# Kernel optimization log

Hardware: AMD Instinct MI355X
Metric: run time of the kernel (lower is better)

Reference implementation:

```python
import jax, jax.numpy as jnp
import numpy as np

N_NODES = 100000
N_EDGES = 600000
N_GRAPHS = 256
K = 5
N_FEAT = 16
N_CLASSES = 4


def setup_inputs() -> dict:
    key = jax.random.key(0)
    ks = jax.random.split(key, 12)
    x = jax.random.normal(ks[0], (N_NODES, N_FEAT), dtype=jnp.float32)
    edge_index = jax.random.randint(ks[1], (2, N_EDGES), 0, N_NODES, dtype=jnp.int32)
    batch = jnp.sort(jax.random.randint(ks[2], (N_NODES,), 0, N_GRAPHS, dtype=jnp.int32))
    s = 0.1
    W11 = jax.random.normal(ks[3], (K, N_FEAT, 64), dtype=jnp.float32) * s
    b11 = jnp.zeros((64,), dtype=jnp.float32)
    W12 = jax.random.normal(ks[4], (K, N_FEAT, 64), dtype=jnp.float32) * s
    b12 = jnp.zeros((64,), dtype=jnp.float32)
    W21 = jax.random.normal(ks[5], (K, 128, 256), dtype=jnp.float32) * s
    b21 = jnp.zeros((256,), dtype=jnp.float32)
    W22 = jax.random.normal(ks[6], (K, 128, 256), dtype=jnp.float32) * s
    b22 = jnp.zeros((256,), dtype=jnp.float32)
    fc_w = jax.random.normal(ks[7], (512, N_CLASSES), dtype=jnp.float32) * s
    fc_b = jnp.zeros((N_CLASSES,), dtype=jnp.float32)
    return {
        "x": x, "edge_index": edge_index, "batch": batch,
        "W11": W11, "b11": b11, "W12": W12, "b12": b12,
        "W21": W21, "b21": b21, "W22": W22, "b22": b22,
        "fc_w": fc_w, "fc_b": fc_b,
    }


def _cheb_norm(src, dst, n_nodes):
    # PyG ChebConv (sym norm, lambda_max=2): L_hat = -D^{-1/2} A D^{-1/2},
    # zero diagonal. Degree computed over source (row) indices.
    deg = jax.ops.segment_sum(jnp.ones_like(src, dtype=jnp.float32), src,
                              num_segments=n_nodes)
    dinv = jnp.where(deg > 0, jax.lax.rsqrt(jnp.maximum(deg, 1.0)), 0.0)
    return -dinv[src] * dinv[dst]


def _cheb_conv(x, src, dst, w_norm, W, b):
    # Chebyshev recursion: Tx0=x, Tx1=L_hat x, Txk = 2 L_hat Tx_{k-1} - Tx_{k-2}
    n = x.shape[0]

    def spmm(h):  # aggregate messages from src at dst
        return jax.ops.segment_sum(h[src] * w_norm[:, None], dst, num_segments=n)

    Tx0 = x
    Tx1 = spmm(x)
    out = jnp.einsum('nf,fo->no', Tx0, W[0]) + jnp.einsum('nf,fo->no', Tx1, W[1])
    for k in range(2, W.shape[0]):
        Tx2 = 2.0 * spmm(Tx1) - Tx0
        out = out + jnp.einsum('nf,fo->no', Tx2, W[k])
        Tx0, Tx1 = Tx1, Tx2
    return out + b


def reference(x, edge_index, batch, W11, b11, W12, b12, W21, b21, W22, b22,
              fc_w, fc_b):
    src, dst = edge_index[0], edge_index[1]
    w_fwd = _cheb_norm(src, dst, N_NODES)
    w_rev = _cheb_norm(dst, src, N_NODES)  # reversed adjacency

    x1 = jax.nn.relu(_cheb_conv(x, src, dst, w_fwd, W11, b11))
    x2 = jax.nn.relu(_cheb_conv(x, dst, src, w_rev, W12, b12))
    h = jnp.concatenate([x1, x2], axis=1)  # [N, 128]

    x1 = jax.nn.relu(_cheb_conv(h, src, dst, w_fwd, W21, b21))
    x2 = jax.nn.relu(_cheb_conv(h, dst, src, w_rev, W22, b22))
    h = jnp.concatenate([x1, x2], axis=1)  # [N, 512]

    # global mean pool over graphs
    sums = jax.ops.segment_sum(h, batch, num_segments=N_GRAPHS)
    cnt = jax.ops.segment_sum(jnp.ones((h.shape[0],), dtype=h.dtype), batch,
                              num_segments=N_GRAPHS)
    pooled = sums / jnp.maximum(cnt, 1.0)[:, None]  # [G, 512]

    logits = pooled @ fc_w + fc_b
    return jax.nn.log_softmax(logits, axis=1)
```

## Files before the change

### kernel.cpp

```cpp
#include <hip/hip_runtime.h>
#include <stdint.h>

#define NNODES 100000
#define NEDGES 600000
#define NGRAPH 256
#define KCH 5
#define F1 16
#define O1 64
#define F2 128
#define O2 256
#define FT1 (KCH * F1)
#define FT2 (KCH * F2)
#define STR2 512
#define KSTEPS 20
#define KS1 3
#define LROW 40
#define LROWD 68
#define NXCD 8

typedef unsigned short ushort_t;
typedef __attribute__((ext_vector_type(8))) short bf16x8;
typedef __attribute__((ext_vector_type(4))) float f32x4;

__device__ __forceinline__ float bflo(unsigned int u) {
    union { unsigned int u; float f; } v; v.u = u << 16; return v.f;
}
__device__ __forceinline__ float bfhi(unsigned int u) {
    union { unsigned int u; float f; } v; v.u = u & 0xFFFF0000u; return v.f;
}
__device__ __forceinline__ unsigned int f2bf(float f) {
    union { float f; unsigned int u; } v; v.f = f;
    return (v.u + 0x7FFFu + ((v.u >> 16) & 1u)) >> 16;
}
__device__ __forceinline__ unsigned int pack2(float lo, float hi) {
    return (f2bf(hi) << 16) | f2bf(lo);
}


__global__ void k_count(const int* __restrict__ src, const int* __restrict__ dst,
                        int* __restrict__ cntDst, int* __restrict__ cntSrc, int E) {
    int e = blockIdx.x * 256 + threadIdx.x;
    if (e < E) {
        atomicAdd(&cntDst[dst[e]], 1);
        atomicAdd(&cntSrc[src[e]], 1);
    }
}

__global__ void k_dinv(const int* __restrict__ cntDst, const int* __restrict__ cntSrc,
                       float* __restrict__ dinvF, float* __restrict__ dinvR, int n) {
    int i = blockIdx.x * 256 + threadIdx.x;
    if (i < n) {
        int cs = cntSrc[i], cd = cntDst[i];
        dinvF[i] = cs > 0 ? rsqrtf((float)cs) : 0.f;
        dinvR[i] = cd > 0 ? rsqrtf((float)cd) : 0.f;
    }
}

__global__ void k_scan1m(const int* __restrict__ inF, int* __restrict__ outF,
                         int* __restrict__ bsF,
                         const int* __restrict__ inR, int* __restrict__ outR,
                         int* __restrict__ bsR, int n, int NB) {
    __shared__ int a[512];
    __shared__ int s[256];
    int b = blockIdx.x;
    const int* in; int* out; int* bs; int lb;
    if (b < NB) { in = inF; out = outF; bs = bsF; lb = b; }
    else        { in = inR; out = outR; bs = bsR; lb = b - NB; }
    int t = threadIdx.x;
    int base = lb * 512;
    a[t]       = (base + t < n)       ? in[base + t]       : 0;
    a[t + 256] = (base + t + 256 < n) ? in[base + t + 256] : 0;
    __syncthreads();
    s[t] = a[2 * t] + a[2 * t + 1];
    __syncthreads();
    for (int off = 1; off < 256; off <<= 1) {
        int v = (t >= off) ? s[t - off] : 0;
        __syncthreads();
        s[t] += v;
        __syncthreads();
    }
    int ep = (t > 0) ? s[t - 1] : 0;
    if (base + 2 * t < n)     out[base + 2 * t]     = ep;
    if (base + 2 * t + 1 < n) out[base + 2 * t + 1] = ep + a[2 * t];
    if (t == 255) bs[lb] = s[255];
}

__global__ void k_scan2m(int* __restrict__ bsF, int* __restrict__ bsR, int nb) {
    __shared__ int s[256];
    int* bs = (blockIdx.x == 0) ? bsF : bsR;
    int t = threadIdx.x;
    s[t] = (t < nb) ? bs[t] : 0;
    __syncthreads();
    for (int off = 1; off < 256; off <<= 1) {
        int v = (t >= off) ? s[t - off] : 0;
        __syncthreads();
        s[t] += v;
        __syncthreads();
    }
    if (t < nb) bs[t] = (t > 0) ? s[t - 1] : 0;
}

__global__ void k_scan3m(int* __restrict__ outF, int* __restrict__ curF,
                         const int* __restrict__ bsF,
                         int* __restrict__ outR, int* __restrict__ curR,
                         const int* __restrict__ bsR, int n, int E, int NB) {
    int b = blockIdx.x;
    int* out; int* cur; const int* bs; int lb;
    if (b < NB) { out = outF; cur = curF; bs = bsF; lb = b; }
    else        { out = outR; cur = curR; bs = bsR; lb = b - NB; }
    int i = lb * 512 + threadIdx.x;
    int add = bs[lb];
    if (i < n)       { int v = out[i] + add;       out[i] = v;       cur[i] = v; }
    if (i + 256 < n) { int v = out[i + 256] + add; out[i + 256] = v; cur[i + 256] = v; }
    if (lb == 0 && threadIdx.x == 0) out[n] = E;
}

__global__ void k_scatter(const int* __restrict__ src, const int* __restrict__ dst,
                          const float* __restrict__ dinvF, const float* __restrict__ dinvR,
                          int* __restrict__ curF, int* __restrict__ curR,
                          int2* __restrict__ edF, int2* __restrict__ edR, int E,
                          int chunk) {
    int c = blockIdx.x & (NXCD - 1);
    int sb = blockIdx.x >> 3;
    int slices = gridDim.x >> 3;
    int lo = c * chunk, hi = lo + chunk;
    for (int e = sb * 256 + threadIdx.x; e < E; e += slices * 256) {
        int s = src[e], d = dst[e];
        if (d >= lo && d < hi) {
            int p = atomicAdd(&curF[d], 1);
            float wf = -dinvF[s] * dinvF[d];
            edF[p] = make_int2(s, __float_as_int(wf));
        }
        if (s >= lo && s < hi) {
            int q = atomicAdd(&curR[s], 1);
            float wr = -dinvR[s] * dinvR[d];
            edR[q] = make_int2(d, __float_as_int(wr));
        }
    }
}

__global__ void k_gstart(const int* __restrict__ batch, int* __restrict__ gstart, int n) {
    int g = blockIdx.x * 64 + threadIdx.x;
    if (g > NGRAPH) return;
    if (g == NGRAPH) { gstart[g] = n; return; }
    int lo = 0, hi = n;
    while (lo < hi) {
        int mid = (lo + hi) >> 1;
        if (batch[mid] < g) lo = mid + 1; else hi = mid;
    }
    gstart[g] = lo;
}


__global__ void k_copyx(const float* __restrict__ x, float* __restrict__ Tx,
                        ushort_t* __restrict__ TxB, int n) {
    int tid = blockIdx.x * 256 + threadIdx.x;
    int r = tid >> 2, c = tid & 3;
    if (r < n) {
        float4 v = *(const float4*)(x + (size_t)r * 16 + c * 4);
        *(float4*)(Tx + (size_t)r * FT1 + c * 4) = v;
        uint2 b;
        b.x = pack2(v.x, v.y);
        b.y = pack2(v.z, v.w);
        *(uint2*)(TxB + (size_t)r * F1 + c * 4) = b;
    }
}

__global__ void k_spmm_f32(const ushort_t* __restrict__ HinB, float* __restrict__ Hout,
                           ushort_t* __restrict__ HoutB,
                           const float* __restrict__ Tx0,
                           const int* __restrict__ off, const int2* __restrict__ ed,
                           int n) {
    int tid = blockIdx.x * 256 + threadIdx.x;
    int r = tid >> 2, c = tid & 3;
    if (r >= n) return;
    int j0 = off[r], j1 = off[r + 1];
    float4 s = {0.f, 0.f, 0.f, 0.f};
    int j = j0;
    for (; j + 4 <= j1; j += 4) {
        int2 e0 = ed[j], e1 = ed[j + 1], e2 = ed[j + 2], e3 = ed[j + 3];
        float wa = __int_as_float(e0.y), wb = __int_as_float(e1.y);
        float wc = __int_as_float(e2.y), wd = __int_as_float(e3.y);
        const uint2 h0 = *(const uint2*)(HinB + (size_t)e0.x * F1 + c * 4);
        const uint2 h1 = *(const uint2*)(HinB + (size_t)e1.x * F1 + c * 4);
        const uint2 h2 = *(const uint2*)(HinB + (size_t)e2.x * F1 + c * 4);
        const uint2 h3 = *(const uint2*)(HinB + (size_t)e3.x * F1 + c * 4);
        s.x = fmaf(wa, bflo(h0.x), s.x); s.y = fmaf(wa, bfhi(h0.x), s.y);
        s.z = fmaf(wa, bflo(h0.y), s.z); s.w = fmaf(wa, bfhi(h0.y), s.w);
        s.x = fmaf(wb, bflo(h1.x), s.x); s.y = fmaf(wb, bfhi(h1.x), s.y);
        s.z = fmaf(wb, bflo(h1.y), s.z); s.w = fmaf(wb, bfhi(h1.y), s.w);
        s.x = fmaf(wc, bflo(h2.x), s.x); s.y = fmaf(wc, bfhi(h2.x), s.y);
        s.z = fmaf(wc, bflo(h2.y), s.z); s.w = fmaf(wc, bfhi(h2.y), s.w);
        s.x = fmaf(wd, bflo(h3.x), s.x); s.y = fmaf(wd, bfhi(h3.x), s.y);
        s.z = fmaf(wd, bflo(h3.y), s.z); s.w = fmaf(wd, bfhi(h3.y), s.w);
    }
    for (; j < j1; ++j) {
        int2 e = ed[j];
        float w2 = __int_as_float(e.y);
        const uint2 h = *(const uint2*)(HinB + (size_t)e.x * F1 + c * 4);
        s.x = fmaf(w2, bflo(h.x), s.x); s.y = fmaf(w2, bfhi(h.x), s.y);
        s.z = fmaf(w2, bflo(h.y), s.z); s.w = fmaf(w2, bfhi(h.y), s.w);
    }
    float4 o;
    if (Tx0) {
        const float4 t0 = *(const float4*)(Tx0 + (size_t)r * FT1 + c * 4);
        o.x = 2.f * s.x - t0.x; o.y = 2.f * s.y - t0.y;
        o.z = 2.f * s.z - t0.z; o.w = 2.f * s.w - t0.w;
    } else {
        o = s;
    }
    *(float4*)(Hout + (size_t)r * FT1 + c * 4) = o;
    if (HoutB) {
        uint2 b;
        b.x = pack2(o.x, o.y);
        b.y = pack2(o.z, o.w);
        *(uint2*)(HoutB + (size_t)r * F1 + c * 4) = b;
    }
}

__global__ void k_spmm_bf(const ushort_t* __restrict__ Hin, ushort_t* __restrict__ Hout,
                          const ushort_t* __restrict__ Tx0,
                          const int* __restrict__ off, const int2* __restrict__ ed,
                          int n) {
    int r = blockIdx.x * 4 + (threadIdx.x >> 6);
    r = __builtin_amdgcn_readfirstlane(r);
    int c = threadIdx.x & 63;
    if (r >= n) return;
    int j0 = __builtin_amdgcn_readfirstlane(off[r]);
    int j1 = __builtin_amdgcn_readfirstlane(off[r + 1]);
    float s0 = 0.f, s1 = 0.f;
    int j = j0;
    int jfull = j0 + ((j1 - j0) & ~7);
    for (; j < jfull; j += 8) {
        float w[8];
        unsigned int h[8];
#pragma unroll
        for (int sl = 0; sl < 8; ++sl) {
            int2 e = ed[j + sl];
            w[sl] = __int_as_float(e.y);
            h[sl] = *(const unsigned int*)(Hin + (size_t)e.x * STR2 + c * 2);
        }
#pragma unroll
        for (int sl = 0; sl < 8; ++sl) {
            s0 = fmaf(bflo(h[sl]), w[sl], s0);
            s1 = fmaf(bfhi(h[sl]), w[sl], s1);
        }
    }
    int rem = j1 - j;
    if (rem) {
        float w[8];
        unsigned int h[8];
#pragma unroll
        for (int sl = 0; sl < 8; ++sl) {
            w[sl] = 0.f; h[sl] = 0u;
            if (sl < rem) {
                int2 e = ed[j + sl];
                w[sl] = __int_as_float(e.y);
                h[sl] = *(const unsigned int*)(Hin + (size_t)e.x * STR2 + c * 2);
            }
        }
#pragma unroll
        for (int sl = 0; sl < 8; ++sl) {
            s0 = fmaf(bflo(h[sl]), w[sl], s0);
            s1 = fmaf(bfhi(h[sl]), w[sl], s1);
        }
    }
    if (Tx0) {
        unsigned int t0 = *(const unsigned int*)(Tx0 + (size_t)r * STR2 + c * 2);
        s0 = 2.f * s0 - bflo(t0);
        s1 = 2.f * s1 - bfhi(t0);
    }
    *(unsigned int*)(Hout + (size_t)r * STR2 + c * 2) = pack2(s0, s1);
}

__global__ void k_packW1m(const float* __restrict__ WF, ushort_t* __restrict__ BpF_,
                          const float* __restrict__ WR, ushort_t* __restrict__ BpR_) {
    int b = blockIdx.x;
    const float* W = (b < 3) ? WF : WR;
    ushort_t* Bp = (b < 3) ? BpF_ : BpR_;
    int tid = ((b < 3) ? b : b - 3) * 256 + threadIdx.x;
    if (tid >= 4 * KS1 * 64) return;
    int lane = tid & 63;
    int ks = (tid >> 6) % KS1;
    int nt = tid / (64 * KS1);
    int k0 = ks * 32 + (lane >> 4) * 8;
    int ncol = nt * 16 + (lane & 15);
    float v[8];
#pragma unroll
    for (int j = 0; j < 8; ++j) {
        int k = k0 + j;
        v[j] = (k < FT1) ? W[(size_t)k * O1 + ncol] : 0.f;
    }
    uint4 o;
    o.x = pack2(v[0], v[1]); o.y = pack2(v[2], v[3]);
    o.z = pack2(v[4], v[5]); o.w = pack2(v[6], v[7]);
    *(uint4*)(Bp + (size_t)tid * 8) = o;
}

__global__ __launch_bounds__(256) void k_gemm1_mfma(
    const float* __restrict__ A, const ushort_t* __restrict__ Bp,
    const float* __restrict__ bias, ushort_t* __restrict__ out, int n) {
    int lane = threadIdx.x & 63;
    int wvi = threadIdx.x >> 6;
    int mrow = lane & 15;
    int quad = lane >> 4;
    int m0w = blockIdx.x * 64 + wvi * 16;
    int row = m0w + mrow;
    int rowc = row < n ? row : n - 1;
    const float* Ar = A + (size_t)rowc * FT1 + quad * 8;

    f32x4 acc[4] = {};
#pragma unroll
    for (int ks = 0; ks < KS1; ++ks) {
        float4 a0 = *(const float4*)(Ar + ks * 32);
        float4 a1 = *(const float4*)(Ar + ks * 32 + 4);
        union { bf16x8 v; unsigned int u[4]; } ua;
        ua.u[0] = pack2(a0.x, a0.y);
        ua.u[1] = pack2(a0.z, a0.w);
        ua.u[2] = pack2(a1.x, a1.y);
        ua.u[3] = pack2(a1.z, a1.w);
#pragma unroll
        for (int nf = 0; nf < 4; ++nf) {
            bf16x8 bfr = *(const bf16x8*)(Bp + ((size_t)(nf * KS1 + ks) * 64 + lane) * 8);
            acc[nf] = __builtin_amdgcn_mfma_f32_16x16x32_bf16(ua.v, bfr, acc[nf], 0, 0, 0);
        }
    }
#pragma unroll
    for (int nf = 0; nf < 4; ++nf) {
        float bb = bias[nf * 16 + mrow];
#pragma unroll
        for (int reg = 0; reg < 4; ++reg) {
            int orow = m0w + quad * 4 + reg;
            if (orow < n)
                out[(size_t)orow * STR2 + nf * 16 + mrow] =
                    (ushort_t)f2bf(fmaxf(acc[nf][reg] + bb, 0.f));
        }
    }
}

__global__ void k_packWm(const float* __restrict__ WF, ushort_t* __restrict__ BpF_,
                         const float* __restrict__ WR, ushort_t* __restrict__ BpR_) {
    int b = blockIdx.x;
    const float* W = (b < 80) ? WF : WR;
    ushort_t* Bp = (b < 80) ? BpF_ : BpR_;
    int tid = ((b < 80) ? b : b - 80) * 256 + threadIdx.x;
    if (tid >= 16 * KSTEPS * 64) return;
    int lane = tid & 63;
    int ks = (tid >> 6) % KSTEPS;
    int nt = tid / (64 * KSTEPS);
    int k0 = ks * 32 + (lane >> 4) * 8;
    int ncol = nt * 16 + (lane & 15);
    float v[8];
#pragma unroll
    for (int j = 0; j < 8; ++j) v[j] = W[(size_t)(k0 + j) * O2 + ncol];
    uint4 o;
    o.x = pack2(v[0], v[1]); o.y = pack2(v[2], v[3]);
    o.z = pack2(v[4], v[5]); o.w = pack2(v[6], v[7]);
    *(uint4*)(Bp + (size_t)tid * 8) = o;
}

__global__ __launch_bounds__(256) void k_spmm4_gemm(
    const ushort_t* __restrict__ Hin,
    const ushort_t* __restrict__ Txc,
    const int* __restrict__ off, const int2* __restrict__ ed,
    const ushort_t* __restrict__ A,
    const ushort_t* __restrict__ Bp,
    const float* __restrict__ bias, float* __restrict__ pooled, int colofs,
    const int* __restrict__ batch, int n) {
    __shared__ ushort_t lds[2][64 * LROW];
    __shared__ unsigned int a4[64 * LROWD];

    int lane = threadIdx.x & 63;
    int wv = threadIdx.x >> 6;
    int m0 = blockIdx.x * 64;

    for (int i = 0; i < 16; ++i) {
        int r = m0 + wv * 16 + i;
        float s0 = 0.f, s1 = 0.f;
        if (r < n) {
            int j0 = __builtin_amdgcn_readfirstlane(off[r]);
            int j1 = __builtin_amdgcn_readfirstlane(off[r + 1]);
            int j = j0;
            int jfull = j0 + ((j1 - j0) & ~7);
            for (; j < jfull; j += 8) {
                float w[8];
                unsigned int h[8];
#pragma unroll
                for (int sl = 0; sl < 8; ++sl) {
                    int2 e = ed[j + sl];
                    w[sl] = __int_as_float(e.y);
                    h[sl] = *(const unsigned int*)(Hin + (size_t)e.x * STR2 + lane * 2);
                }
#pragma unroll
                for (int sl = 0; sl < 8; ++sl) {
                    s0 = fmaf(bflo(h[sl]), w[sl], s0);
                    s1 = fmaf(bfhi(h[sl]), w[sl], s1);
                }
            }
            int rem = j1 - j;
            if (rem) {
                float w[8];
                unsigned int h[8];
#pragma unroll
                for (int sl = 0; sl < 8; ++sl) {
                    w[sl] = 0.f; h[sl] = 0u;
                    if (sl < rem) {
                        int2 e = ed[j + sl];
                        w[sl] = __int_as_float(e.y);
                        h[sl] = *(const unsigned int*)(Hin + (size_t)e.x * STR2 + lane * 2);
                    }
                }
#pragma unroll
                for (int sl = 0; sl < 8; ++sl) {
                    s0 = fmaf(bflo(h[sl]), w[sl], s0);
                    s1 = fmaf(bfhi(h[sl]), w[sl], s1);
                }
            }
            unsigned int t0 = *(const unsigned int*)(Txc + (size_t)r * STR2 + lane * 2);
            s0 = 2.f * s0 - bflo(t0);
            s1 = 2.f * s1 - bfhi(t0);
        }
        a4[(wv * 16 + i) * LROWD + lane] = pack2(s0, s1);
    }
    __syncthreads();

    int mrow = lane & 15;
    int quad = lane >> 4;
    int srow = threadIdx.x >> 2;
    int sc = threadIdx.x & 3;

    const ushort_t* Ag = A + (size_t)(m0 + srow) * STR2 + sc * 8;
    const ushort_t* Bbase = Bp + ((size_t)(wv * 4) * KSTEPS * 64 + lane) * 8;
    int sidx = srow * LROW + sc * 8;

    f32x4 acc[4][4] = {};
    uint4 nxt;
    bf16x8 bcur[4], bnxt[4];
    {
        uint4 c0 = *(const uint4*)(Ag);
        *(uint4*)&lds[0][sidx] = c0;
        nxt = *(const uint4*)(Ag + 32);
#pragma unroll
        for (int nf = 0; nf < 4; ++nf)
            bcur[nf] = *(const bf16x8*)(Bbase + ((size_t)nf * KSTEPS) * 512);
    }

    for (int ks = 0; ks < KSTEPS; ++ks) {
        __syncthreads();
        if (ks + 1 < 16)
            *(uint4*)&lds[(ks + 1) & 1][sidx] = nxt;
        if (ks + 2 < 16)
            nxt = *(const uint4*)(Ag + (ks + 2) * 32);
        if (ks + 1 < KSTEPS) {
#pragma unroll
            for (int nf = 0; nf < 4; ++nf)
                bnxt[nf] = *(const bf16x8*)(Bbase + ((size_t)nf * KSTEPS + ks + 1) * 512);
        }
        bf16x8 af[4];
        if (ks < 16) {
            const ushort_t* lbuf = &lds[ks & 1][0];
#pragma unroll
            for (int mf = 0; mf < 4; ++mf)
                af[mf] = *(const bf16x8*)(lbuf + (mf * 16 + mrow) * LROW + quad * 8);
        } else {
            int kk = ks - 16;
#pragma unroll
            for (int mf = 0; mf < 4; ++mf)
                af[mf] = *(const bf16x8*)(a4 + (size_t)(mf * 16 + mrow) * LROWD +
                                          kk * 16 + quad * 4);
        }
#pragma unroll
        for (int mf = 0; mf < 4; ++mf)
#pragma unroll
            for (int nf = 0; nf < 4; ++nf)
                acc[mf][nf] = __builtin_amdgcn_mfma_f32_16x16x32_bf16(
                    af[mf], bcur[nf], acc[mf][nf], 0, 0, 0);
#pragma unroll
        for (int nf = 0; nf < 4; ++nf) bcur[nf] = bnxt[nf];
    }

    float bcol[4];
#pragma unroll
    for (int nf = 0; nf < 4; ++nf) bcol[nf] = bias[wv * 64 + nf * 16 + mrow];

#pragma unroll
    for (int mf = 0; mf < 4; ++mf) {
        int t0 = m0 + mf * 16;
        if (t0 >= n) break;
        int te = (t0 + 15 < n) ? t0 + 15 : n - 1;
        int r0 = t0 + quad * 4;
        if (batch[t0] == batch[te]) {
            int g = batch[t0];
#pragma unroll
            for (int nf = 0; nf < 4; ++nf) {
                float s = 0.f;
#pragma unroll
                for (int reg = 0; reg < 4; ++reg) {
                    float v = fmaxf(acc[mf][nf][reg] + bcol[nf], 0.f);
                    if (r0 + reg < n) s += v;
                }
                s += __shfl_xor(s, 16, 64);
                s += __shfl_xor(s, 32, 64);
                if (quad == 0)
                    atomicAdd(pooled + (size_t)g * 512 + colofs + wv * 64 + nf * 16 + mrow, s);
            }
        } else {
            int gb[4];
#pragma unroll
            for (int reg = 0; reg < 4; ++reg)
                gb[reg] = batch[(r0 + reg < n) ? r0 + reg : n - 1];
#pragma unroll
            for (int nf = 0; nf < 4; ++nf) {
                int col = colofs + wv * 64 + nf * 16 + mrow;
                float run = 0.f;
                int g = gb[0];
                bool any = false;
#pragma unroll
                for (int reg = 0; reg < 4; ++reg) {
                    int row = r0 + reg;
                    if (row >= n) break;
                    float v = fmaxf(acc[mf][nf][reg] + bcol[nf], 0.f);
                    if (gb[reg] != g) {
                        atomicAdd(pooled + (size_t)g * 512 + col, run);
                        run = 0.f;
                        g = gb[reg];
                    }
                    run += v;
                    any = true;
                }
                if (any) atomicAdd(pooled + (size_t)g * 512 + col, run);
            }
        }
    }
}

__global__ void k_logits(const float* __restrict__ pooled, const int* __restrict__ gstart,
                         const float* __restrict__ fcw, const float* __restrict__ fcb,
                         float* __restrict__ out) {
    int g = blockIdx.x;
    int l = threadIdx.x;
    int cnt = gstart[g + 1] - gstart[g];
    float inv = 1.f / (float)(cnt > 1 ? cnt : 1);
    float lg0 = 0.f, lg1 = 0.f, lg2 = 0.f, lg3 = 0.f;
    for (int f = l; f < 512; f += 64) {
        float p = pooled[g * 512 + f] * inv;
        const float4 wv4 = *(const float4*)(fcw + f * 4);
        lg0 = fmaf(p, wv4.x, lg0);
        lg1 = fmaf(p, wv4.y, lg1);
        lg2 = fmaf(p, wv4.z, lg2);
        lg3 = fmaf(p, wv4.w, lg3);
    }
#pragma unroll
    for (int o = 32; o > 0; o >>= 1) {
        lg0 += __shfl_down(lg0, o, 64);
        lg1 += __shfl_down(lg1, o, 64);
        lg2 += __shfl_down(lg2, o, 64);
        lg3 += __shfl_down(lg3, o, 64);
    }
    if (l == 0) {
        float lg[4] = {lg0 + fcb[0], lg1 + fcb[1], lg2 + fcb[2], lg3 + fcb[3]};
        float m = fmaxf(fmaxf(lg[0], lg[1]), fmaxf(lg[2], lg[3]));
        float s = 0.f;
#pragma unroll
        for (int o = 0; o < 4; ++o) s += expf(lg[o] - m);
        float lsum = logf(s);
#pragma unroll
        for (int o = 0; o < 4; ++o) out[g * 4 + o] = lg[o] - m - lsum;
    }
}


extern "C" void kernel_launch(void* const* d_in, const int* in_sizes, int n_in,
                              void* d_out, int out_size, void* d_ws, size_t ws_size,
                              hipStream_t stream) {
    const float* x   = (const float*)d_in[0];
    const int* ei    = (const int*)d_in[1];
    const int* batch = (const int*)d_in[2];
    const float* W11 = (const float*)d_in[3];
    const float* b11 = (const float*)d_in[4];
    const float* W12 = (const float*)d_in[5];
    const float* b12 = (const float*)d_in[6];
    const float* W21 = (const float*)d_in[7];
    const float* b21 = (const float*)d_in[8];
    const float* W22 = (const float*)d_in[9];
    const float* b22 = (const float*)d_in[10];
    const float* fcw = (const float*)d_in[11];
    const float* fcb = (const float*)d_in[12];
    float* out = (float*)d_out;

    const int N = in_sizes[0] / F1;
    const int E = in_sizes[1] / 2;
    const int* src = ei;
    const int* dst = ei + E;

    char* w = (char*)d_ws;
    size_t pos = 0;
    auto alloc = [&](size_t bytes) -> void* {
        void* p = w + pos;
        pos += (bytes + 255) & ~(size_t)255;
        return p;
    };
    int* cur_f   = (int*)alloc((size_t)N * 4);
    int* cur_r   = (int*)alloc((size_t)N * 4);
    int* off_f   = (int*)alloc((size_t)(N + 1) * 4);
    int* off_r   = (int*)alloc((size_t)(N + 1) * 4);
    float* dinvF = (float*)alloc((size_t)N * 4);
    float* dinvR = (float*)alloc((size_t)N * 4);
    int2* ed_f   = (int2*)alloc((size_t)E * 8);
    int2* ed_r   = (int2*)alloc((size_t)E * 8);
    int* blks_f  = (int*)alloc(1024);
    int* blks_r  = (int*)alloc(1024);
    int* gstart  = (int*)alloc((NGRAPH + 1) * 4);
    float* pooled = (float*)alloc((size_t)NGRAPH * 512 * 4);
    ushort_t* BpF = (ushort_t*)alloc((size_t)FT2 * O2 * 2);
    ushort_t* BpR = (ushort_t*)alloc((size_t)FT2 * O2 * 2);
    ushort_t* Bp1F = (ushort_t*)alloc((size_t)4 * KS1 * 64 * 8 * 2);
    ushort_t* Bp1R = (ushort_t*)alloc((size_t)4 * KS1 * 64 * 8 * 2);
    float* TxAll1 = (float*)alloc(((size_t)N * FT1 + 256) * 4);
    ushort_t* TxB1 = (ushort_t*)alloc((size_t)KCH * N * F1 * 2);
    ushort_t* TxAll2 = (ushort_t*)alloc((size_t)(N + 64) * STR2 * 2);

    (void)hipMemsetAsync(cur_f, 0, (size_t)N * 4, stream);
    (void)hipMemsetAsync(cur_r, 0, (size_t)N * 4, stream);
    (void)hipMemsetAsync(pooled, 0, (size_t)NGRAPH * 512 * 4, stream);

    int gE = (E + 255) / 256, gN = (N + 255) / 256;
    k_count<<<gE, 256, 0, stream>>>(src, dst, cur_f, cur_r, E);
    k_dinv<<<gN, 256, 0, stream>>>(cur_f, cur_r, dinvF, dinvR, N);

    int NB = (N + 511) / 512;
    k_scan1m<<<2 * NB, 256, 0, stream>>>(cur_f, off_f, blks_f, cur_r, off_r, blks_r, N, NB);
    k_scan2m<<<2, 256, 0, stream>>>(blks_f, blks_r, NB);
    k_scan3m<<<2 * NB, 256, 0, stream>>>(off_f, cur_f, blks_f, off_r, cur_r, blks_r, N, E, NB);
    int chunk = (N + NXCD - 1) / NXCD;
    k_scatter<<<NXCD * 256, 256, 0, stream>>>(src, dst, dinvF, dinvR, cur_f, cur_r,
                                              ed_f, ed_r, E, chunk);
    k_gstart<<<5, 64, 0, stream>>>(batch, gstart, N);
    k_packWm<<<160, 256, 0, stream>>>(W21, BpF, W22, BpR);
    k_packW1m<<<6, 256, 0, stream>>>(W11, Bp1F, W12, Bp1R);

    k_copyx<<<(N * 4 + 255) / 256, 256, 0, stream>>>(x, TxAll1, TxB1, N);
    int gs1 = (N * 4 + 255) / 256;
    int gg1 = (N + 63) / 64;
    auto C1 = [&](int k) { return TxAll1 + k * F1; };
    auto B1 = [&](int k) { return TxB1 + (size_t)k * N * F1; };
    k_spmm_f32<<<gs1, 256, 0, stream>>>(B1(0), C1(1), B1(1), nullptr, off_f, ed_f, N);
    k_spmm_f32<<<gs1, 256, 0, stream>>>(B1(1), C1(2), B1(2), C1(0), off_f, ed_f, N);
    k_spmm_f32<<<gs1, 256, 0, stream>>>(B1(2), C1(3), B1(3), C1(1), off_f, ed_f, N);
    k_spmm_f32<<<gs1, 256, 0, stream>>>(B1(3), C1(4), nullptr, C1(2), off_f, ed_f, N);
    k_gemm1_mfma<<<gg1, 256, 0, stream>>>(TxAll1, Bp1F, b11, TxAll2, N);
    k_spmm_f32<<<gs1, 256, 0, stream>>>(B1(0), C1(1), B1(1), nullptr, off_r, ed_r, N);
    k_spmm_f32<<<gs1, 256, 0, stream>>>(B1(1), C1(2), B1(2), C1(0), off_r, ed_r, N);
    k_spmm_f32<<<gs1, 256, 0, stream>>>(B1(2), C1(3), B1(3), C1(1), off_r, ed_r, N);
    k_spmm_f32<<<gs1, 256, 0, stream>>>(B1(3), C1(4), nullptr, C1(2), off_r, ed_r, N);
    k_gemm1_mfma<<<gg1, 256, 0, stream>>>(TxAll1, Bp1R, b12, TxAll2 + O1, N);

    int gs2 = (N + 3) / 4;
    auto C2 = [&](int k) { return TxAll2 + k * F2; };
    int gg = (N + 63) / 64;
    k_spmm_bf<<<gs2, 256, 0, stream>>>(C2(0), C2(1), nullptr, off_f, ed_f, N);
    k_spmm_bf<<<gs2, 256, 0, stream>>>(C2(1), C2(2), C2(0), off_f, ed_f, N);
    k_spmm_bf<<<gs2, 256, 0, stream>>>(C2(2), C2(3), C2(1), off_f, ed_f, N);
    k_spmm4_gemm<<<gg, 256, 0, stream>>>(C2(3), C2(2), off_f, ed_f, TxAll2, BpF,
                                         b21, pooled, 0, batch, N);
    k_spmm_bf<<<gs2, 256, 0, stream>>>(C2(0), C2(1), nullptr, off_r, ed_r, N);
    k_spmm_bf<<<gs2, 256, 0, stream>>>(C2(1), C2(2), C2(0), off_r, ed_r, N);
    k_spmm_bf<<<gs2, 256, 0, stream>>>(C2(2), C2(3), C2(1), off_r, ed_r, N);
    k_spmm4_gemm<<<gg, 256, 0, stream>>>(C2(3), C2(2), off_r, ed_r, TxAll2, BpR,
                                         b22, pooled, 256, batch, N);

    k_logits<<<NGRAPH, 64, 0, stream>>>(pooled, gstart, fcw, fcb, out);
}
```

Baseline: 854.8 us.

## Batch forward and reverse Chebyshev branches into dual-direction kernel launches

Forward and reverse Chebyshev branches now run in shared launches: blockIdx selects direction, which doubles the grid and halves the launch count. Layer-2 features move to separate H (stride 128) and per-direction C buffers, and the fused spmm4+gemm becomes a plain spmm followed by a GEMM that reads H and C. Layer-1 spmm now gathers fp32 directly instead of a bf16 shadow copy. This adds workspace (a second C buffer) and a serial fallback path, and drops the spmm4-in-GEMM fusion, which costs an extra write and read of Tx4.

```diff
diff --git a/kernel.cpp b/kernel.cpp
--- a/kernel.cpp
+++ b/kernel.cpp
@@ -1,8 +1,6 @@
 #include <hip/hip_runtime.h>
 #include <stdint.h>
 
-#define NNODES 100000
-#define NEDGES 600000
 #define NGRAPH 256
 #define KCH 5
 #define F1 16
@@ -11,11 +9,11 @@
 #define O2 256
 #define FT1 (KCH * F1)
 #define FT2 (KCH * F2)
-#define STR2 512
+#define STRH 128
+#define STRC 512
 #define KSTEPS 20
 #define KS1 3
 #define LROW 40
-#define LROWD 68
 #define NXCD 8
 
 typedef unsigned short ushort_t;
@@ -152,26 +150,30 @@
 }
 
 
-__global__ void k_copyx(const float* __restrict__ x, float* __restrict__ Tx,
-                        ushort_t* __restrict__ TxB, int n) {
+__global__ void k_copyx(const float* __restrict__ x, float* __restrict__ TxF,
+                        float* __restrict__ TxR, int n) {
     int tid = blockIdx.x * 256 + threadIdx.x;
     int r = tid >> 2, c = tid & 3;
     if (r < n) {
         float4 v = *(const float4*)(x + (size_t)r * 16 + c * 4);
-        *(float4*)(Tx + (size_t)r * FT1 + c * 4) = v;
-        uint2 b;
-        b.x = pack2(v.x, v.y);
-        b.y = pack2(v.z, v.w);
-        *(uint2*)(TxB + (size_t)r * F1 + c * 4) = b;
-    }
-}
-
-__global__ void k_spmm_f32(const ushort_t* __restrict__ HinB, float* __restrict__ Hout,
-                           ushort_t* __restrict__ HoutB,
-                           const float* __restrict__ Tx0,
-                           const int* __restrict__ off, const int2* __restrict__ ed,
-                           int n) {
-    int tid = blockIdx.x * 256 + threadIdx.x;
+        *(float4*)(TxF + (size_t)r * FT1 + c * 4) = v;
+        if (TxR) *(float4*)(TxR + (size_t)r * FT1 + c * 4) = v;
+    }
+}
+
+__global__ void k_spmm_f32d(const float* __restrict__ HinF, float* __restrict__ HoutF,
+                            const float* __restrict__ Tx0F,
+                            const float* __restrict__ HinR, float* __restrict__ HoutR,
+                            const float* __restrict__ Tx0R,
+                            const int* __restrict__ offF, const int2* __restrict__ edF,
+                            const int* __restrict__ offR, const int2* __restrict__ edR,
+                            int n, int half) {
+    int b = blockIdx.x;
+    const float* Hin; float* Hout; const float* Tx0;
+    const int* off; const int2* ed; int lb;
+    if (b < half) { Hin = HinF; Hout = HoutF; Tx0 = Tx0F; off = offF; ed = edF; lb = b; }
+    else          { Hin = HinR; Hout = HoutR; Tx0 = Tx0R; off = offR; ed = edR; lb = b - half; }
+    int tid = lb * 256 + threadIdx.x;
     int r = tid >> 2, c = tid & 3;
     if (r >= n) return;
     int j0 = off[r], j1 = off[r + 1];
@@ -181,25 +183,20 @@
         int2 e0 = ed[j], e1 = ed[j + 1], e2 = ed[j + 2], e3 = ed[j + 3];
         float wa = __int_as_float(e0.y), wb = __int_as_float(e1.y);
         float wc = __int_as_float(e2.y), wd = __int_as_float(e3.y);
-        const uint2 h0 = *(const uint2*)(HinB + (size_t)e0.x * F1 + c * 4);
-        const uint2 h1 = *(const uint2*)(HinB + (size_t)e1.x * F1 + c * 4);
-        const uint2 h2 = *(const uint2*)(HinB + (size_t)e2.x * F1 + c * 4);
-        const uint2 h3 = *(const uint2*)(HinB + (size_t)e3.x * F1 + c * 4);
-        s.x = fmaf(wa, bflo(h0.x), s.x); s.y = fmaf(wa, bfhi(h0.x), s.y);
-        s.z = fmaf(wa, bflo(h0.y), s.z); s.w = fmaf(wa, bfhi(h0.y), s.w);
-        s.x = fmaf(wb, bflo(h1.x), s.x); s.y = fmaf(wb, bfhi(h1.x), s.y);
-        s.z = fmaf(wb, bflo(h1.y), s.z); s.w = fmaf(wb, bfhi(h1.y), s.w);
-        s.x = fmaf(wc, bflo(h2.x), s.x); s.y = fmaf(wc, bfhi(h2.x), s.y);
-        s.z = fmaf(wc, bflo(h2.y), s.z); s.w = fmaf(wc, bfhi(h2.y), s.w);
-        s.x = fmaf(wd, bflo(h3.x), s.x); s.y = fmaf(wd, bfhi(h3.x), s.y);
-        s.z = fmaf(wd, bflo(h3.y), s.z); s.w = fmaf(wd, bfhi(h3.y), s.w);
+        const float4 h0 = *(const float4*)(Hin + (size_t)e0.x * FT1 + c * 4);
+        const float4 h1 = *(const float4*)(Hin + (size_t)e1.x * FT1 + c * 4);
+        const float4 h2 = *(const float4*)(Hin + (size_t)e2.x * FT1 + c * 4);
+        const float4 h3 = *(const float4*)(Hin + (size_t)e3.x * FT1 + c * 4);
+        s.x += wa * h0.x; s.y += wa * h0.y; s.z += wa * h0.z; s.w += wa * h0.w;
+        s.x += wb * h1.x; s.y += wb * h1.y; s.z += wb * h1.z; s.w += wb * h1.w;
+        s.x += wc * h2.x; s.y += wc * h2.y; s.z += wc * h2.z; s.w += wc * h2.w;
+        s.x += wd * h3.x; s.y += wd * h3.y; s.z += wd * h3.z; s.w += wd * h3.w;
     }
     for (; j < j1; ++j) {
         int2 e = ed[j];
         float w2 = __int_as_float(e.y);
-        const uint2 h = *(const uint2*)(HinB + (size_t)e.x * F1 + c * 4);
-        s.x = fmaf(w2, bflo(h.x), s.x); s.y = fmaf(w2, bfhi(h.x), s.y);
-        s.z = fmaf(w2, bflo(h.y), s.z); s.w = fmaf(w2, bfhi(h.y), s.w);
+        const float4 h = *(const float4*)(Hin + (size_t)e.x * FT1 + c * 4);
+        s.x += w2 * h.x; s.y += w2 * h.y; s.z += w2 * h.z; s.w += w2 * h.w;
     }
     float4 o;
     if (Tx0) {
@@ -210,19 +207,22 @@
         o = s;
     }
     *(float4*)(Hout + (size_t)r * FT1 + c * 4) = o;
-    if (HoutB) {
-        uint2 b;
-        b.x = pack2(o.x, o.y);
-        b.y = pack2(o.z, o.w);
-        *(uint2*)(HoutB + (size_t)r * F1 + c * 4) = b;
-    }
-}
-
-__global__ void k_spmm_bf(const ushort_t* __restrict__ Hin, ushort_t* __restrict__ Hout,
-                          const ushort_t* __restrict__ Tx0,
-                          const int* __restrict__ off, const int2* __restrict__ ed,
-                          int n) {
-    int r = blockIdx.x * 4 + (threadIdx.x >> 6);
+}
+
+__global__ void k_spmm_bfd(const ushort_t* __restrict__ HinF, ushort_t* __restrict__ HoutF,
+                           const ushort_t* __restrict__ Tx0F,
+                           const ushort_t* __restrict__ HinR, ushort_t* __restrict__ HoutR,
+                           const ushort_t* __restrict__ Tx0R,
+                           int strIn, int strOut, int strT0,
+                           const int* __restrict__ offF, const int2* __restrict__ edF,
+                           const int* __restrict__ offR, const int2* __restrict__ edR,
+                           int n, int half) {
+    int b = blockIdx.x;
+    const ushort_t* Hin; ushort_t* Hout; const ushort_t* Tx0;
+    const int* off; const int2* ed; int lb;
+    if (b < half) { Hin = HinF; Hout = HoutF; Tx0 = Tx0F; off = offF; ed = edF; lb = b; }
+    else          { Hin = HinR; Hout = HoutR; Tx0 = Tx0R; off = offR; ed = edR; lb = b - half; }
+    int r = lb * 4 + (threadIdx.x >> 6);
     r = __builtin_amdgcn_readfirstlane(r);
     int c = threadIdx.x & 63;
     if (r >= n) return;
@@ -238,7 +238,7 @@
         for (int sl = 0; sl < 8; ++sl) {
             int2 e = ed[j + sl];
             w[sl] = __int_as_float(e.y);
-            h[sl] = *(const unsigned int*)(Hin + (size_t)e.x * STR2 + c * 2);
+            h[sl] = *(const unsigned int*)(Hin + (size_t)e.x * strIn + c * 2);
         }
 #pragma unroll
         for (int sl = 0; sl < 8; ++sl) {
@@ -256,7 +256,7 @@
             if (sl < rem) {
                 int2 e = ed[j + sl];
                 w[sl] = __int_as_float(e.y);
-                h[sl] = *(const unsigned int*)(Hin + (size_t)e.x * STR2 + c * 2);
+                h[sl] = *(const unsigned int*)(Hin + (size_t)e.x * strIn + c * 2);
             }
         }
 #pragma unroll
@@ -266,11 +266,11 @@
         }
     }
     if (Tx0) {
-        unsigned int t0 = *(const unsigned int*)(Tx0 + (size_t)r * STR2 + c * 2);
+        unsigned int t0 = *(const unsigned int*)(Tx0 + (size_t)r * strT0 + c * 2);
         s0 = 2.f * s0 - bflo(t0);
         s1 = 2.f * s1 - bfhi(t0);
     }
-    *(unsigned int*)(Hout + (size_t)r * STR2 + c * 2) = pack2(s0, s1);
+    *(unsigned int*)(Hout + (size_t)r * strOut + c * 2) = pack2(s0, s1);
 }
 
 __global__ void k_packW1m(const float* __restrict__ WF, ushort_t* __restrict__ BpF_,
@@ -297,14 +297,21 @@
     *(uint4*)(Bp + (size_t)tid * 8) = o;
 }
 
-__global__ __launch_bounds__(256) void k_gemm1_mfma(
-    const float* __restrict__ A, const ushort_t* __restrict__ Bp,
-    const float* __restrict__ bias, ushort_t* __restrict__ out, int n) {
+__global__ __launch_bounds__(256) void k_gemm1d(
+    const float* __restrict__ AF, const ushort_t* __restrict__ BpF_,
+    const float* __restrict__ bF,
+    const float* __restrict__ AR, const ushort_t* __restrict__ BpR_,
+    const float* __restrict__ bR,
+    ushort_t* __restrict__ H, int n, int half) {
+    int b = blockIdx.x;
+    const float* A; const ushort_t* Bp; const float* bias; int colb; int lb;
+    if (b < half) { A = AF; Bp = BpF_; bias = bF; colb = 0;  lb = b; }
+    else          { A = AR; Bp = BpR_; bias = bR; colb = O1; lb = b - half; }
     int lane = threadIdx.x & 63;
     int wvi = threadIdx.x >> 6;
     int mrow = lane & 15;
     int quad = lane >> 4;
-    int m0w = blockIdx.x * 64 + wvi * 16;
+    int m0w = lb * 64 + wvi * 16;
     int row = m0w + mrow;
     int rowc = row < n ? row : n - 1;
     const float* Ar = A + (size_t)rowc * FT1 + quad * 8;
@@ -332,7 +339,7 @@
         for (int reg = 0; reg < 4; ++reg) {
             int orow = m0w + quad * 4 + reg;
             if (orow < n)
-                out[(size_t)orow * STR2 + nf * 16 + mrow] =
+                H[(size_t)orow * STRH + colb + nf * 16 + mrow] =
                     (ushort_t)f2bf(fmaxf(acc[nf][reg] + bb, 0.f));
         }
     }
@@ -359,116 +366,64 @@
     *(uint4*)(Bp + (size_t)tid * 8) = o;
 }
 
-__global__ __launch_bounds__(256) void k_spmm4_gemm(
-    const ushort_t* __restrict__ Hin,
-    const ushort_t* __restrict__ Txc,
-    const int* __restrict__ off, const int2* __restrict__ ed,
-    const ushort_t* __restrict__ A,
-    const ushort_t* __restrict__ Bp,
-    const float* __restrict__ bias, float* __restrict__ pooled, int colofs,
-    const int* __restrict__ batch, int n) {
+__global__ __launch_bounds__(256) void k_gemm2d(
+    const ushort_t* __restrict__ H,
+    const ushort_t* __restrict__ CFp, const ushort_t* __restrict__ BpF_,
+    const float* __restrict__ bF,
+    const ushort_t* __restrict__ CRp, const ushort_t* __restrict__ BpR_,
+    const float* __restrict__ bR,
+    float* __restrict__ pooled, const int* __restrict__ batch, int n, int half) {
     __shared__ ushort_t lds[2][64 * LROW];
-    __shared__ unsigned int a4[64 * LROWD];
+
+    int b = blockIdx.x;
+    const ushort_t* C; const ushort_t* Bp; const float* bias; int colofs; int lb;
+    if (b < half) { C = CFp; Bp = BpF_; bias = bF; colofs = 0;   lb = b; }
+    else          { C = CRp; Bp = BpR_; bias = bR; colofs = 256; lb = b - half; }
 
     int lane = threadIdx.x & 63;
     int wv = threadIdx.x >> 6;
-    int m0 = blockIdx.x * 64;
-
-    for (int i = 0; i < 16; ++i) {
-        int r = m0 + wv * 16 + i;
-        float s0 = 0.f, s1 = 0.f;
-        if (r < n) {
-            int j0 = __builtin_amdgcn_readfirstlane(off[r]);
-            int j1 = __builtin_amdgcn_readfirstlane(off[r + 1]);
-            int j = j0;
-            int jfull = j0 + ((j1 - j0) & ~7);
-            for (; j < jfull; j += 8) {
-                float w[8];
-                unsigned int h[8];
-#pragma unroll
-                for (int sl = 0; sl < 8; ++sl) {
-                    int2 e = ed[j + sl];
-                    w[sl] = __int_as_float(e.y);
-                    h[sl] = *(const unsigned int*)(Hin + (size_t)e.x * STR2 + lane * 2);
-                }
-#pragma unroll
-                for (int sl = 0; sl < 8; ++sl) {
-                    s0 = fmaf(bflo(h[sl]), w[sl], s0);
-                    s1 = fmaf(bfhi(h[sl]), w[sl], s1);
-                }
-            }
-            int rem = j1 - j;
-            if (rem) {
-                float w[8];
-                unsigned int h[8];
-#pragma unroll
-                for (int sl = 0; sl < 8; ++sl) {
-                    w[sl] = 0.f; h[sl] = 0u;
-                    if (sl < rem) {
-                        int2 e = ed[j + sl];
-                        w[sl] = __int_as_float(e.y);
-                        h[sl] = *(const unsigned int*)(Hin + (size_t)e.x * STR2 + lane * 2);
-                    }
-                }
-#pragma unroll
-                for (int sl = 0; sl < 8; ++sl) {
-                    s0 = fmaf(bflo(h[sl]), w[sl], s0);
-                    s1 = fmaf(bfhi(h[sl]), w[sl], s1);
-                }
-            }
-            unsigned int t0 = *(const unsigned int*)(Txc + (size_t)r * STR2 + lane * 2);
-            s0 = 2.f * s0 - bflo(t0);
-            s1 = 2.f * s1 - bfhi(t0);
-        }
-        a4[(wv * 16 + i) * LROWD + lane] = pack2(s0, s1);
-    }
-    __syncthreads();
-
+    int m0 = lb * 64;
     int mrow = lane & 15;
     int quad = lane >> 4;
     int srow = threadIdx.x >> 2;
     int sc = threadIdx.x & 3;
 
-    const ushort_t* Ag = A + (size_t)(m0 + srow) * STR2 + sc * 8;
+    const ushort_t* AgH = H + (size_t)(m0 + srow) * STRH + sc * 8;
+    const ushort_t* AgC = C + (size_t)(m0 + srow) * STRC + sc * 8;
     const ushort_t* Bbase = Bp + ((size_t)(wv * 4) * KSTEPS * 64 + lane) * 8;
     int sidx = srow * LROW + sc * 8;
 
     f32x4 acc[4][4] = {};
     uint4 nxt;
     bf16x8 bcur[4], bnxt[4];
-    {
-        uint4 c0 = *(const uint4*)(Ag);
-        *(uint4*)&lds[0][sidx] = c0;
-        nxt = *(const uint4*)(Ag + 32);
-#pragma unroll
-        for (int nf = 0; nf < 4; ++nf)
-            bcur[nf] = *(const bf16x8*)(Bbase + ((size_t)nf * KSTEPS) * 512);
-    }
+
+    auto aload = [&](int ks) {
+        return (ks < 4) ? *(const uint4*)(AgH + ks * 32)
+                        : *(const uint4*)(AgC + (ks - 4) * 32);
+    };
+
+    *(uint4*)&lds[0][sidx] = aload(0);
+    nxt = aload(1);
+#pragma unroll
+    for (int nf = 0; nf < 4; ++nf)
+        bcur[nf] = *(const bf16x8*)(Bbase + ((size_t)nf * KSTEPS) * 512);
 
     for (int ks = 0; ks < KSTEPS; ++ks) {
         __syncthreads();
-        if (ks + 1 < 16)
+        if (ks + 1 < KSTEPS)
             *(uint4*)&lds[(ks + 1) & 1][sidx] = nxt;
-        if (ks + 2 < 16)
-            nxt = *(const uint4*)(Ag + (ks + 2) * 32);
+        if (ks + 2 < KSTEPS)
+            nxt = aload(ks + 2);
         if (ks + 1 < KSTEPS) {
 #pragma unroll
             for (int nf = 0; nf < 4; ++nf)
                 bnxt[nf] = *(const bf16x8*)(Bbase + ((size_t)nf * KSTEPS + ks + 1) * 512);
         }
         bf16x8 af[4];
-        if (ks < 16) {
-            const ushort_t* lbuf = &lds[ks & 1][0];
-#pragma unroll
-            for (int mf = 0; mf < 4; ++mf)
-                af[mf] = *(const bf16x8*)(lbuf + (mf * 16 + mrow) * LROW + quad * 8);
-        } else {
-            int kk = ks - 16;
-#pragma unroll
-            for (int mf = 0; mf < 4; ++mf)
-                af[mf] = *(const bf16x8*)(a4 + (size_t)(mf * 16 + mrow) * LROWD +
-                                          kk * 16 + quad * 4);
-        }
+        const ushort_t* lbuf = &lds[ks & 1][0];
+#pragma unroll
+        for (int mf = 0; mf < 4; ++mf)
+            af[mf] = *(const bf16x8*)(lbuf + (mf * 16 + mrow) * LROW + quad * 8);
 #pragma unroll
         for (int mf = 0; mf < 4; ++mf)
 #pragma unroll
@@ -616,9 +571,18 @@
     ushort_t* BpR = (ushort_t*)alloc((size_t)FT2 * O2 * 2);
     ushort_t* Bp1F = (ushort_t*)alloc((size_t)4 * KS1 * 64 * 8 * 2);
     ushort_t* Bp1R = (ushort_t*)alloc((size_t)4 * KS1 * 64 * 8 * 2);
-    float* TxAll1 = (float*)alloc(((size_t)N * FT1 + 256) * 4);
-    ushort_t* TxB1 = (ushort_t*)alloc((size_t)KCH * N * F1 * 2);
-    ushort_t* TxAll2 = (ushort_t*)alloc((size_t)(N + 64) * STR2 * 2);
+    ushort_t* H  = (ushort_t*)alloc((size_t)(N + 64) * STRH * 2);
+    ushort_t* CF = (ushort_t*)alloc((size_t)(N + 64) * STRC * 2);
+    float* Tx1F = (float*)alloc(((size_t)N * FT1 + 256) * 4);
+    size_t serialNeed = pos;
+    size_t crOff = (size_t)((char*)Tx1F - w);
+    size_t crBytes = (size_t)(N + 64) * STRC * 2;
+    float* Tx1R = (float*)alloc(((size_t)N * FT1 + 256) * 4);
+    if (pos < crOff + crBytes) pos = crOff + crBytes;
+    size_t dualNeed = pos;
+    bool dual = (ws_size >= dualNeed) && (ws_size >= serialNeed);
+    ushort_t* CR = dual ? (ushort_t*)(w + crOff) : CF;
+    if (!dual) Tx1R = Tx1F;
 
     (void)hipMemsetAsync(cur_f, 0, (size_t)N * 4, stream);
     (void)hipMemsetAsync(cur_r, 0, (size_t)N * 4, stream);
@@ -639,35 +603,111 @@
     k_packWm<<<160, 256, 0, stream>>>(W21, BpF, W22, BpR);
     k_packW1m<<<6, 256, 0, stream>>>(W11, Bp1F, W12, Bp1R);
 
-    k_copyx<<<(N * 4 + 255) / 256, 256, 0, stream>>>(x, TxAll1, TxB1, N);
     int gs1 = (N * 4 + 255) / 256;
     int gg1 = (N + 63) / 64;
-    auto C1 = [&](int k) { return TxAll1 + k * F1; };
-    auto B1 = [&](int k) { return TxB1 + (size_t)k * N * F1; };
-    k_spmm_f32<<<gs1, 256, 0, stream>>>(B1(0), C1(1), B1(1), nullptr, off_f, ed_f, N);
-    k_spmm_f32<<<gs1, 256, 0, stream>>>(B1(1), C1(2), B1(2), C1(0), off_f, ed_f, N);
-    k_spmm_f32<<<gs1, 256, 0, stream>>>(B1(2), C1(3), B1(3), C1(1), off_f, ed_f, N);
-    k_spmm_f32<<<gs1, 256, 0, stream>>>(B1(3), C1(4), nullptr, C1(2), off_f, ed_f, N);
-    k_gemm1_mfma<<<gg1, 256, 0, stream>>>(TxAll1, Bp1F, b11, TxAll2, N);
-    k_spmm_f32<<<gs1, 256, 0, stream>>>(B1(0), C1(1), B1(1), nullptr, off_r, ed_r, N);
-    k_spmm_f32<<<gs1, 256, 0, stream>>>(B1(1), C1(2), B1(2), C1(0), off_r, ed_r, N);
-    k_spmm_f32<<<gs1, 256, 0, stream>>>(B1(2), C1(3), B1(3), C1(1), off_r, ed_r, N);
-    k_spmm_f32<<<gs1, 256, 0, stream>>>(B1(3), C1(4), nullptr, C1(2), off_r, ed_r, N);
-    k_gemm1_mfma<<<gg1, 256, 0, stream>>>(TxAll1, Bp1R, b12, TxAll2 + O1, N);
-
     int gs2 = (N + 3) / 4;
-    auto C2 = [&](int k) { return TxAll2 + k * F2; };
     int gg = (N + 63) / 64;
-    k_spmm_bf<<<gs2, 256, 0, stream>>>(C2(0), C2(1), nullptr, off_f, ed_f, N);
-    k_spmm_bf<<<gs2, 256, 0, stream>>>(C2(1), C2(2), C2(0), off_f, ed_f, N);
-    k_spmm_bf<<<gs2, 256, 0, stream>>>(C2(2), C2(3), C2(1), off_f, ed_f, N);
-    k_spmm4_gemm<<<gg, 256, 0, stream>>>(C2(3), C2(2), off_f, ed_f, TxAll2, BpF,
-                                         b21, pooled, 0, batch, N);
-    k_spmm_bf<<<gs2, 256, 0, stream>>>(C2(0), C2(1), nullptr, off_r, ed_r, N);
-    k_spmm_bf<<<gs2, 256, 0, stream>>>(C2(1), C2(2), C2(0), off_r, ed_r, N);
-    k_spmm_bf<<<gs2, 256, 0, stream>>>(C2(2), C2(3), C2(1), off_r, ed_r, N);
-    k_spmm4_gemm<<<gg, 256, 0, stream>>>(C2(3), C2(2), off_r, ed_r, TxAll2, BpR,
-                                         b22, pooled, 256, batch, N);
+    auto CFc = [&](int k) { return Tx1F + k * F1; };
+    auto CRc = [&](int k) { return Tx1R + k * F1; };
+    auto CT = [&](ushort_t* C, int t) { return C + (t - 1) * F2; };
+
+    if (dual) {
+        k_copyx<<<(N * 4 + 255) / 256, 256, 0, stream>>>(x, Tx1F, Tx1R, N);
+        k_spmm_f32d<<<2 * gs1, 256, 0, stream>>>(CFc(0), CFc(1), nullptr,
+                                                 CRc(0), CRc(1), nullptr,
+                                                 off_f, ed_f, off_r, ed_r, N, gs1);
+        k_spmm_f32d<<<2 * gs1, 256, 0, stream>>>(CFc(1), CFc(2), CFc(0),
+                                                 CRc(1), CRc(2), CRc(0),
+                                                 off_f, ed_f, off_r, ed_r, N, gs1);
+        k_spmm_f32d<<<2 * gs1, 256, 0, stream>>>(CFc(2), CFc(3), CFc(1),
+                                                 CRc(2), CRc(3), CRc(1),
+                                                 off_f, ed_f, off_r, ed_r, N, gs1);
+        k_spmm_f32d<<<2 * gs1, 256, 0, stream>>>(CFc(3), CFc(4), CFc(2),
+                                                 CRc(3), CRc(4), CRc(2),
+                                                 off_f, ed_f, off_r, ed_r, N, gs1);
+        k_gemm1d<<<2 * gg1, 256, 0, stream>>>(Tx1F, Bp1F, b11, Tx1R, Bp1R, b12,
+                                              H, N, gg1);
+        k_spmm_bfd<<<2 * gs2, 256, 0, stream>>>(H, CT(CF, 1), nullptr,
+                                                H, CT(CR, 1), nullptr,
+                                                STRH, STRC, 0,
+                                                off_f, ed_f, off_r, ed_r, N, gs2);
+        k_spmm_bfd<<<2 * gs2, 256, 0, stream>>>(CT(CF, 1), CT(CF, 2), H,
+                                                CT(CR, 1), CT(CR, 2), H,
+                                                STRC, STRC, STRH,
+                                                off_f, ed_f, off_r, ed_r, N, gs2);
+        k_spmm_bfd<<<2 * gs2, 256, 0, stream>>>(CT(CF, 2), CT(CF, 3), CT(CF, 1),
+                                                CT(CR, 2), CT(CR, 3), CT(CR, 1),
+                                                STRC, STRC, STRC,
+                                                off_f, ed_f, off_r, ed_r, N, gs2);
+        k_spmm_bfd<<<2 * gs2, 256, 0, stream>>>(CT(CF, 3), CT(CF, 4), CT(CF, 2),
+                                                CT(CR, 3), CT(CR, 4), CT(CR, 2),
+                                                STRC, STRC, STRC,
+                                                off_f, ed_f, off_r, ed_r, N, gs2);
+        k_gemm2d<<<2 * gg, 256, 0, stream>>>(H, CF, BpF, b21, CR, BpR, b22,
+                                             pooled, batch, N, gg);
+    } else {
+        k_copyx<<<(N * 4 + 255) / 256, 256, 0, stream>>>(x, Tx1F, nullptr, N);
+        k_spmm_f32d<<<gs1, 256, 0, stream>>>(CFc(0), CFc(1), nullptr,
+                                             CFc(0), CFc(1), nullptr,
+                                             off_f, ed_f, off_f, ed_f, N, gs1);
+        k_spmm_f32d<<<gs1, 256, 0, stream>>>(CFc(1), CFc(2), CFc(0),
+                                             CFc(1), CFc(2), CFc(0),
+                                             off_f, ed_f, off_f, ed_f, N, gs1);
+        k_spmm_f32d<<<gs1, 256, 0, stream>>>(CFc(2), CFc(3), CFc(1),
+                                             CFc(2), CFc(3), CFc(1),
+                                             off_f, ed_f, off_f, ed_f, N, gs1);
+        k_spmm_f32d<<<gs1, 256, 0, stream>>>(CFc(3), CFc(4), CFc(2),
+                                             CFc(3), CFc(4), CFc(2),
+                                             off_f, ed_f, off_f, ed_f, N, gs1);
+        k_gemm1d<<<gg1, 256, 0, stream>>>(Tx1F, Bp1F, b11, Tx1F, Bp1R, b12, H, N, gg1);
+        k_spmm_f32d<<<gs1, 256, 0, stream>>>(CFc(0), CFc(1), nullptr,
+                                             CFc(0), CFc(1), nullptr,
+                                             off_r, ed_r, off_r, ed_r, N, 0);
+        k_spmm_f32d<<<gs1, 256, 0, stream>>>(CFc(1), CFc(2), CFc(0),
+                                             CFc(1), CFc(2), CFc(0),
+                                             off_r, ed_r, off_r, ed_r, N, 0);
+        k_spmm_f32d<<<gs1, 256, 0, stream>>>(CFc(2), CFc(3), CFc(1),
+                                             CFc(2), CFc(3), CFc(1),
+                                             off_r, ed_r, off_r, ed_r, N, 0);
+        k_spmm_f32d<<<gs1, 256, 0, stream>>>(CFc(3), CFc(4), CFc(2),
+                                             CFc(3), CFc(4), CFc(2),
+                                             off_r, ed_r, off_r, ed_r, N, 0);
+        k_gemm1d<<<gg1, 256, 0, stream>>>(Tx1F, Bp1F, b11, Tx1F, Bp1R, b12, H, N, 0);
+        k_spmm_bfd<<<gs2, 256, 0, stream>>>(H, CT(CF, 1), nullptr, H, CT(CF, 1), nullptr,
+                                            STRH, STRC, 0,
+                                            off_f, ed_f, off_f, ed_f, N, gs2);
+        k_spmm_bfd<<<gs2, 256, 0, stream>>>(CT(CF, 1), CT(CF, 2), H,
+                                            CT(CF, 1), CT(CF, 2), H,
+                                            STRC, STRC, STRH,
+                                            off_f, ed_f, off_f, ed_f, N, gs2);
+        k_spmm_bfd<<<gs2, 256, 0, stream>>>(CT(CF, 2), CT(CF, 3), CT(CF, 1),
+                                            CT(CF, 2), CT(CF, 3), CT(CF, 1),
+                                            STRC, STRC, STRC,
+                                            off_f, ed_f, off_f, ed_f, N, gs2);
+        k_spmm_bfd<<<gs2, 256, 0, stream>>>(CT(CF, 3), CT(CF, 4), CT(CF, 2),
+                                            CT(CF, 3), CT(CF, 4), CT(CF, 2),
+                                            STRC, STRC, STRC,
+                                            off_f, ed_f, off_f, ed_f, N, gs2);
+        k_gemm2d<<<gg, 256, 0, stream>>>(H, CF, BpF, b21, CF, BpR, b22,
+                                         pooled, batch, N, gg);
+        k_spmm_bfd<<<gs2, 256, 0, stream>>>(H, CT(CF, 1), nullptr, H, CT(CF, 1), nullptr,
+                                            STRH, STRC, 0,
+                                            off_r, ed_r, off_r, ed_r, N, 0);
+        k_spmm_bfd<<<gs2, 256, 0, stream>>>(CT(CF, 1), CT(CF, 2), H,
+                                            CT(CF, 1), CT(CF, 2), H,
+                                            STRC, STRC, STRH,
+                                            off_r, ed_r, off_r, ed_r, N, 0);
+        k_spmm_bfd<<<gs2, 256, 0, stream>>>(CT(CF, 2), CT(CF, 3), CT(CF, 1),
+                                            CT(CF, 2), CT(CF, 3), CT(CF, 1),
+                                            STRC, STRC, STRC,
+                                            off_r, ed_r, off_r, ed_r, N, 0);
+        k_spmm_bfd<<<gs2, 256, 0, stream>>>(CT(CF, 3), CT(CF, 4), CT(CF, 2),
+                                            CT(CF, 3), CT(CF, 4), CT(CF, 2),
+                                            STRC, STRC, STRC,
+                                            off_r, ed_r, off_r, ed_r, N, 0);
+        k_gemm2d<<<gg, 256, 0, stream>>>(H, CF, BpF, b21, CF, BpR, b22,
+                                         pooled, batch, N, 0);
+    }
 
     k_logits<<<NGRAPH, 64, 0, stream>>>(pooled, gstart, fcw, fcb, out);
 }
```

New measurement: 738.4 us. 1.16x faster.
